# Kernel optimization log

Measured on AMD Instinct MI355X. Metric: run time of the kernel, lower is better.

Reference implementation:

```python
import jax, jax.numpy as jnp
import numpy as np

WIDTH = 16
HID = 512
NHEADS = 8
DK = HID // NHEADS
NLAYERS = 2
NHIGHWAY = 2
B = 4
S = 1024
PAD = S + 2 * WIDTH  # padded sequence length


def setup_inputs() -> dict:
    key = jax.random.key(0)
    ks = jax.random.split(key, 10)
    sc = 0.02
    f32 = jnp.float32
    return {
        "inputs": jax.random.normal(ks[0], (B, S, HID), f32),
        "masks": jnp.ones((B, S), jnp.int32),
        # 4 linears (q,k,v,out) per attention, torch Linear layout [out,in]
        "fw_lin_w": sc * jax.random.normal(ks[1], (NLAYERS, 4, HID, HID), f32),
        "fw_lin_b": jnp.zeros((NLAYERS, 4, HID), f32),
        "bw_lin_w": sc * jax.random.normal(ks[2], (NLAYERS, 4, HID, HID), f32),
        "bw_lin_b": jnp.zeros((NLAYERS, 4, HID), f32),
        # Highway: Linear(H, 2H); [:H]=nonlinear part, [H:]=gate (gate bias init 1)
        "fw_hw_w": sc * jax.random.normal(ks[3], (NLAYERS, NHIGHWAY, 2 * HID, HID), f32),
        "fw_hw_b": jnp.zeros((NLAYERS, NHIGHWAY, 2 * HID), f32).at[:, :, HID:].set(1.0),
        "bw_hw_w": sc * jax.random.normal(ks[4], (NLAYERS, NHIGHWAY, 2 * HID, HID), f32),
        "bw_hw_b": jnp.zeros((NLAYERS, NHIGHWAY, 2 * HID), f32).at[:, :, HID:].set(1.0),
        # learned boundary paddings, [width, hidden] per layer
        "fw_pad": sc * jax.random.normal(ks[5], (NLAYERS, WIDTH, HID), f32),
        "bw_pad": sc * jax.random.normal(ks[6], (NLAYERS, WIDTH, HID), f32),
        # relative-position weight vectors, [width+1] per layer
        "fw_rel": sc * jax.random.normal(ks[7], (NLAYERS, WIDTH + 1), f32),
        "bw_rel": sc * jax.random.normal(ks[8], (NLAYERS, WIDTH + 1), f32),
    }


def _band_masks():
    i = jnp.arange(PAD)[:, None]
    j = jnp.arange(PAD)[None, :]
    mf = (j <= i) & (j >= i - WIDTH - 1)          # causal band, width+2 wide
    mb = (j >= i) & (j <= i + WIDTH + 1)          # flipped (anticausal) band
    return mf, mb


def _mha(x, w, b, mask):
    # x: [B, PAD, HID]; w: [4, HID, HID]; b: [4, HID]
    def heads(t):
        return t.reshape(B, PAD, NHEADS, DK).transpose(0, 2, 1, 3)  # bhpd
    q = heads(x @ w[0].T + b[0])
    k = heads(x @ w[1].T + b[1])
    v = heads(x @ w[2].T + b[2])
    scores = jnp.einsum('bhqd,bhkd->bhqk', q, k) / np.sqrt(DK).astype(np.float32)
    scores = jnp.where(mask[None, None], scores, jnp.float32(-1e9))
    p = jax.nn.softmax(scores, axis=-1)
    o = jnp.einsum('bhqk,bhkd->bhqd', p, v)
    o = o.transpose(0, 2, 1, 3).reshape(B, PAD, HID)
    return o @ w[3].T + b[3]


def _highway(x, w, b):
    for i in range(NHIGHWAY):
        proj = x @ w[i].T + b[i]
        nonlin = jax.nn.relu(proj[..., :HID])
        gate = jax.nn.sigmoid(proj[..., HID:])
        x = gate * x + (1.0 - gate) * nonlin
    return x


def _rel(x, w, offset):
    # sum_k w[k] * x[:, offset+k : offset+k+S, :]  (width+1=17 fixed taps)
    out = w[0] * jax.lax.dynamic_slice_in_dim(x, offset, S, 1)
    for k in range(1, WIDTH + 1):
        out = out + w[k] * jax.lax.dynamic_slice_in_dim(x, offset + k, S, 1)
    return out


def _forward(inputs, fw_lin_w, fw_lin_b, bw_lin_w, bw_lin_b,
             fw_hw_w, fw_hw_b, bw_hw_w, bw_hw_b,
             fw_pad, bw_pad, fw_rel, bw_rel):
    mf, mb = _band_masks()
    f = inputs
    bk = inputs
    outs = []
    for l in range(NLAYERS):
        fp = jnp.broadcast_to(fw_pad[l][None], (B, WIDTH, HID))
        bp = jnp.broadcast_to(bw_pad[l][None], (B, WIDTH, HID))
        f_padded = jnp.concatenate([fp, f, bp], axis=1)    # [B, PAD, HID]
        b_padded = jnp.concatenate([fp, bk, bp], axis=1)
        fa = _mha(f_padded, fw_lin_w[l], fw_lin_b[l], mf)
        ba = _mha(b_padded, bw_lin_w[l], bw_lin_b[l], mb)
        # per-step: out[t] = attn[t+width] + rel-position windowed combination
        fo = fa[:, WIDTH:WIDTH + S, :] + _rel(fa, fw_rel[l], 0)
        bo = ba[:, WIDTH:WIDTH + S, :] + _rel(ba, bw_rel[l], WIDTH)
        f = _highway(fo, fw_hw_w[l], fw_hw_b[l])
        bk = _highway(bo, bw_hw_w[l], bw_hw_b[l])
        outs.append(jnp.concatenate([f, bk], axis=-1))
    return jnp.stack(outs, axis=0)  # [NLAYERS, B, S, 2*HID]


def reference(inputs, masks, fw_lin_w, fw_lin_b, bw_lin_w, bw_lin_b,
              fw_hw_w, fw_hw_b, bw_hw_w, bw_hw_b,
              fw_pad, bw_pad, fw_rel, bw_rel):
    # masks is accepted (as in the torch signature) but unused in the body
    return _forward(inputs, fw_lin_w, fw_lin_b, bw_lin_w, bw_lin_b,
                    fw_hw_w, fw_hw_b, bw_hw_w, bw_hw_b,
                    fw_pad, bw_pad, fw_rel, bw_rel)
```

## Files before the change

kernel.cpp:

```cpp
#include <hip/hip_runtime.h>

using s8 = __attribute__((ext_vector_type(8))) short;
using f4 = __attribute__((ext_vector_type(4))) float;

constexpr int WIDTH   = 16;
constexpr int HID     = 512;
constexpr int NHEADS  = 8;
constexpr int DK      = 64;
constexpr int NLAYERS = 2;
constexpr int NHW     = 2;
constexpr int B       = 4;
constexpr int S       = 1024;
constexpr int PAD     = S + 2 * WIDTH;
constexpr int RS      = 1024;
constexpr int K2      = 1024;

__device__ inline unsigned short f2bf(float x) {
    union { float f; unsigned u; } c; c.f = x;
    unsigned r = c.u + 0x7fffu + ((c.u >> 16) & 1u);
    return (unsigned short)(r >> 16);
}
__device__ inline float bf2f(unsigned short h) {
    union { float f; unsigned u; } c; c.u = ((unsigned)h) << 16; return c.f;
}
__device__ inline void split2(float x, unsigned short& h, unsigned short& l) {
    h = f2bf(x);
    l = f2bf(x - bf2f(h));
}
__device__ inline void store_split4(unsigned short* dst, float4 v) {
    unsigned short h[4], l[4];
    split2(v.x, h[0], l[0]); split2(v.y, h[1], l[1]);
    split2(v.z, h[2], l[2]); split2(v.w, h[3], l[3]);
    uint2 hp, lp;
    hp.x = h[0] | ((unsigned)h[1] << 16); hp.y = h[2] | ((unsigned)h[3] << 16);
    lp.x = l[0] | ((unsigned)l[1] << 16); lp.y = l[2] | ((unsigned)l[3] << 16);
    *(uint2*)(dst)       = hp;
    *(uint2*)(dst + 512) = lp;
}

__global__ __launch_bounds__(256) void build_pad_split(
    const float* __restrict__ src0, const float* __restrict__ src1,
    const float* __restrict__ front, const float* __restrict__ back,
    unsigned short* __restrict__ d0, unsigned short* __restrict__ d1)
{
    const float* x = blockIdx.z ? src1 : src0;
    unsigned short* xp2 = blockIdx.z ? d1 : d0;
    int idx = blockIdx.x * 256 + threadIdx.x;
    int c4 = idx & 127;
    int rest = idx >> 7;
    int p = rest % PAD;
    int b = rest / PAD;
    float4 val;
    if (p < WIDTH) {
        val = *(const float4*)(front + (size_t)p * HID + c4 * 4);
    } else if (p < WIDTH + S) {
        val = *(const float4*)(x + ((size_t)b * S + (p - WIDTH)) * HID + c4 * 4);
    } else {
        val = *(const float4*)(back + (size_t)(p - WIDTH - S) * HID + c4 * 4);
    }
    store_split4(xp2 + (size_t)(b * PAD + p) * RS + c4 * 4, val);
}

__global__ __launch_bounds__(256) void conv_w(
    const float* __restrict__ s0, const float* __restrict__ s1,
    unsigned short* __restrict__ w0, unsigned short* __restrict__ w1)
{
    const float* src = blockIdx.z ? s1 : s0;
    unsigned short* dst = blockIdx.z ? w1 : w0;
    int idx = blockIdx.x * 256 + threadIdx.x;
    int c4 = idx & 127;
    int r  = idx >> 7;
    float4 v = *(const float4*)(src + (size_t)r * HID + c4 * 4);
    store_split4(dst + (size_t)r * RS + c4 * 4, v);
}

__global__ __launch_bounds__(256) void conv_all(
    const float* __restrict__ fw_lin_w, const float* __restrict__ bw_lin_w,
    const float* __restrict__ fw_hw_w,  const float* __restrict__ bw_hw_w,
    unsigned short* __restrict__ w2all)
{
    int idx = blockIdx.x * 256 + threadIdx.x;
    int c4 = idx & 127;
    int r  = idx >> 7;
    int l  = r >> 12;
    int rr = r & 4095;
    const float* lin = blockIdx.z ? bw_lin_w : fw_lin_w;
    const float* hw  = blockIdx.z ? bw_hw_w  : fw_hw_w;
    const float* src;
    size_t drow;
    if (rr < 2048) {
        src  = lin + ((size_t)l * 2048 + rr) * HID;
        drow = (size_t)blockIdx.z * 8192 + (size_t)l * 4096 + rr;
    } else {
        int sub  = rr - 2048;
        int i_hw = sub >> 10;
        int rr2  = sub & 1023;
        int c    = rr2 & 511;
        int is_g = rr2 >> 9;
        int p    = ((c >> 4) << 5) + (c & 15) + (is_g << 4);
        src  = hw + ((size_t)l * 2048 + sub) * HID;
        drow = (size_t)blockIdx.z * 8192 + (size_t)l * 4096 + 2048 + (i_hw << 10) + p;
    }
    float4 v = *(const float4*)(src + c4 * 4);
    store_split4(w2all + drow * RS + c4 * 4, v);
}

__global__ __launch_bounds__(256) void gemm_split(
    const unsigned short* __restrict__ A0, const unsigned short* __restrict__ B0,
    const float* __restrict__ bias0, float* __restrict__ C0,
    const unsigned short* __restrict__ A1, const unsigned short* __restrict__ B1,
    const float* __restrict__ bias1, float* __restrict__ C1,
    int N)
{
    const unsigned short* A  = blockIdx.z ? A1 : A0;
    const unsigned short* Bw = blockIdx.z ? B1 : B0;
    const float* bias        = blockIdx.z ? bias1 : bias0;
    float* C                 = blockIdx.z ? C1 : C0;

    __shared__ unsigned short Als[128 * 32];
    __shared__ unsigned short Bls[128 * 32];

    const int tid  = threadIdx.x;
    const int wave = tid >> 6;
    const int lane = tid & 63;
    const int bm = blockIdx.y * 128;
    const int bn = blockIdx.x * 128;
    const int wm = (wave >> 1) * 64;
    const int wn = (wave & 1) * 64;

    const int c0 = wave * 2, c1 = wave * 2 + 1;
    const int lr = lane >> 2;
    const int kg = ((lane & 3) + (lr >> 1)) & 3;
    const int sr0 = c0 * 16 + lr;
    const int sr1 = c1 * 16 + lr;
    const int sc  = kg * 8;
    const unsigned short* Ag0 = A  + (size_t)(bm + sr0) * RS + sc;
    const unsigned short* Ag1 = A  + (size_t)(bm + sr1) * RS + sc;
    const unsigned short* Bg0 = Bw + (size_t)(bn + sr0) * RS + sc;
    const unsigned short* Bg1 = Bw + (size_t)(bn + sr1) * RS + sc;
    const int ls0 = c0 * 512;
    const int ls1 = c1 * 512;

    const int fr = lane & 15;
    const int q  = lane >> 4;
    const int rslot = (4 * fr + ((q - (fr >> 1)) & 3)) * 8;

    f4 acc[4][4] = {};

    for (int k0 = 0; k0 < K2; k0 += 32) {
        const int aoff = k0;
        const int boff = (k0 < 512) ? k0 : (k0 - 512);
        __builtin_amdgcn_global_load_lds(
            (const __attribute__((address_space(1))) void*)(Ag0 + aoff),
            (__attribute__((address_space(3))) void*)&Als[ls0], 16, 0, 0);
        __builtin_amdgcn_global_load_lds(
            (const __attribute__((address_space(1))) void*)(Ag1 + aoff),
            (__attribute__((address_space(3))) void*)&Als[ls1], 16, 0, 0);
        __builtin_amdgcn_global_load_lds(
            (const __attribute__((address_space(1))) void*)(Bg0 + boff),
            (__attribute__((address_space(3))) void*)&Bls[ls0], 16, 0, 0);
        __builtin_amdgcn_global_load_lds(
            (const __attribute__((address_space(1))) void*)(Bg1 + boff),
            (__attribute__((address_space(3))) void*)&Bls[ls1], 16, 0, 0);
        __syncthreads();

        s8 a[4], b[4];
        #pragma unroll
        for (int i = 0; i < 4; ++i)
            a[i] = *(const s8*)&Als[((wm >> 4) + i) * 512 + rslot];
        #pragma unroll
        for (int j = 0; j < 4; ++j)
            b[j] = *(const s8*)&Bls[((wn >> 4) + j) * 512 + rslot];
        #pragma unroll
        for (int i = 0; i < 4; ++i)
            #pragma unroll
            for (int j = 0; j < 4; ++j)
                acc[i][j] = __builtin_amdgcn_mfma_f32_16x16x32_bf16(
                    a[i], b[j], acc[i][j], 0, 0, 0);
        __syncthreads();
    }

    const int col = lane & 15;
    const int rb  = (lane >> 4) * 4;
    #pragma unroll
    for (int j = 0; j < 4; ++j) {
        float bj = bias[bn + wn + j * 16 + col];
        #pragma unroll
        for (int i = 0; i < 4; ++i) {
            size_t base = (size_t)(bm + wm + i * 16 + rb) * N + (bn + wn + j * 16 + col);
            #pragma unroll
            for (int r = 0; r < 4; ++r)
                C[base + (size_t)r * N] = acc[i][j][r] + bj;
        }
    }
}

__global__ __launch_bounds__(256) void gemm_hw_fused(
    const unsigned short* __restrict__ A0, const unsigned short* __restrict__ B0,
    const float* __restrict__ hwb0, unsigned short* __restrict__ o2_0,
    float* __restrict__ dst0, float* __restrict__ osl0,
    const unsigned short* __restrict__ A1, const unsigned short* __restrict__ B1,
    const float* __restrict__ hwb1, unsigned short* __restrict__ o2_1,
    float* __restrict__ dst1, float* __restrict__ osl1,
    int first)
{
    const unsigned short* A  = blockIdx.z ? A1 : A0;
    const unsigned short* Bw = blockIdx.z ? B1 : B0;
    const float* hwb         = blockIdx.z ? hwb1 : hwb0;
    unsigned short* o2       = blockIdx.z ? o2_1 : o2_0;
    float* dstf              = blockIdx.z ? dst1 : dst0;
    float* osl               = blockIdx.z ? osl1 : osl0;

    __shared__ unsigned short Als[128 * 32];
    __shared__ unsigned short Bls[128 * 32];

    const int tid  = threadIdx.x;
    const int wave = tid >> 6;
    const int lane = tid & 63;
    const int bm = blockIdx.y * 128;
    const int bn = blockIdx.x * 128;
    const int wm = (wave >> 1) * 64;
    const int wn = (wave & 1) * 64;

    const int c0 = wave * 2, c1 = wave * 2 + 1;
    const int lr = lane >> 2;
    const int kg = ((lane & 3) + (lr >> 1)) & 3;
    const int sr0 = c0 * 16 + lr;
    const int sr1 = c1 * 16 + lr;
    const int sc  = kg * 8;
    const unsigned short* Ag0 = A  + (size_t)(bm + sr0) * RS + sc;
    const unsigned short* Ag1 = A  + (size_t)(bm + sr1) * RS + sc;
    const unsigned short* Bg0 = Bw + (size_t)(bn + sr0) * RS + sc;
    const unsigned short* Bg1 = Bw + (size_t)(bn + sr1) * RS + sc;
    const int ls0 = c0 * 512;
    const int ls1 = c1 * 512;

    const int fr = lane & 15;
    const int q  = lane >> 4;
    const int rslot = (4 * fr + ((q - (fr >> 1)) & 3)) * 8;

    f4 acc[4][4] = {};

    for (int k0 = 0; k0 < K2; k0 += 32) {
        const int aoff = k0;
        const int boff = (k0 < 512) ? k0 : (k0 - 512);
        __builtin_amdgcn_global_load_lds(
            (const __attribute__((address_space(1))) void*)(Ag0 + aoff),
            (__attribute__((address_space(3))) void*)&Als[ls0], 16, 0, 0);
        __builtin_amdgcn_global_load_lds(
            (const __attribute__((address_space(1))) void*)(Ag1 + aoff),
            (__attribute__((address_space(3))) void*)&Als[ls1], 16, 0, 0);
        __builtin_amdgcn_global_load_lds(
            (const __attribute__((address_space(1))) void*)(Bg0 + boff),
            (__attribute__((address_space(3))) void*)&Bls[ls0], 16, 0, 0);
        __builtin_amdgcn_global_load_lds(
            (const __attribute__((address_space(1))) void*)(Bg1 + boff),
            (__attribute__((address_space(3))) void*)&Bls[ls1], 16, 0, 0);
        __syncthreads();

        s8 a[4], b[4];
        #pragma unroll
        for (int i = 0; i < 4; ++i)
            a[i] = *(const s8*)&Als[((wm >> 4) + i) * 512 + rslot];
        #pragma unroll
        for (int j = 0; j < 4; ++j)
            b[j] = *(const s8*)&Bls[((wn >> 4) + j) * 512 + rslot];
        #pragma unroll
        for (int i = 0; i < 4; ++i)
            #pragma unroll
            for (int j = 0; j < 4; ++j)
                acc[i][j] = __builtin_amdgcn_mfma_f32_16x16x32_bf16(
                    a[i], b[j], acc[i][j], 0, 0, 0);
        __syncthreads();
    }

    const int col = lane & 15;
    const int rb  = (lane >> 4) * 4;
    #pragma unroll
    for (int jp = 0; jp < 2; ++jp) {
        const int cc = ((bn + wn) >> 1) + jp * 16 + col;
        const float bnl = hwb[cc];
        const float bg  = hwb[512 + cc];
        #pragma unroll
        for (int i = 0; i < 4; ++i) {
            #pragma unroll
            for (int r = 0; r < 4; ++r) {
                const int row = bm + wm + i * 16 + rb + r;
                float nl = acc[i][2 * jp][r] + bnl;
                float g  = acc[i][2 * jp + 1][r] + bg;
                float xv = bf2f(A[(size_t)row * RS + cc])
                         + bf2f(A[(size_t)row * RS + cc + 512]);
                float sg = 1.f / (1.f + __expf(-g));
                float o  = sg * xv + (1.f - sg) * fmaxf(nl, 0.f);
                if (first) {
                    unsigned short hh, ll; split2(o, hh, ll);
                    o2[(size_t)row * RS + cc]       = hh;
                    o2[(size_t)row * RS + cc + 512] = ll;
                } else {
                    dstf[(size_t)row * HID + cc]      = o;
                    osl[(size_t)row * (2 * HID) + cc] = o;
                }
            }
        }
    }
}

__global__ __launch_bounds__(256) void banded_attn(
    const float* __restrict__ Q0, const float* __restrict__ Q1,
    unsigned short* __restrict__ O0, unsigned short* __restrict__ O1,
    int dir0)
{
    const float* QKV = blockIdx.z ? Q1 : Q0;
    unsigned short* O2 = blockIdx.z ? O1 : O0;
    int backward = dir0 + blockIdx.z;

    int w    = blockIdx.x * 4 + (threadIdx.x >> 6);
    int lane = threadIdx.x & 63;
    int i  = w % PAD;
    int bh = w / PAD;
    int h  = bh & (NHEADS - 1);
    int b  = bh / NHEADS;

    int jlo, n;
    if (backward) { jlo = i; n = min(WIDTH + 2, PAD - i); }
    else          { jlo = max(0, i - WIDTH - 1); n = i - jlo + 1; }

    const int s = lane >> 4;
    const int d = lane & 15;
    const size_t rowbase = (size_t)(b * PAD) * 1536;
    const int colq = h * DK;

    float4 q4 = *(const float4*)(QKV + rowbase + (size_t)i * 1536 + colq + 4 * d);

    float sc[5];
    #pragma unroll
    for (int m = 0; m < 5; ++m) {
        int t  = 4 * m + s;
        int tc = t < n ? t : n - 1;
        float4 kv = *(const float4*)(QKV + rowbase + (size_t)(jlo + tc) * 1536
                                     + 512 + colq + 4 * d);
        float p = q4.x * kv.x + q4.y * kv.y + q4.z * kv.z + q4.w * kv.w;
        p += __shfl_xor(p, 1);
        p += __shfl_xor(p, 2);
        p += __shfl_xor(p, 4);
        p += __shfl_xor(p, 8);
        sc[m] = p * 0.125f;
    }

    float sv[WIDTH + 2];
    #pragma unroll
    for (int t = 0; t < WIDTH + 2; ++t) {
        float v = __shfl(sc[t >> 2], (t & 3) << 4);
        sv[t] = (t < n) ? v : -1e30f;
    }
    float mx = sv[0];
    #pragma unroll
    for (int t = 1; t < WIDTH + 2; ++t) mx = fmaxf(mx, sv[t]);
    float denom = 0.f;
    #pragma unroll
    for (int t = 0; t < WIDTH + 2; ++t) { sv[t] = __expf(sv[t] - mx); denom += sv[t]; }
    float inv = 1.0f / denom;

    float od0 = 0.f, od1 = 0.f;
    #pragma unroll
    for (int t = 0; t < WIDTH + 2; t += 2) {
        int tc0 = t     < n ? t     : n - 1;
        int tc1 = t + 1 < n ? t + 1 : n - 1;
        od0 += sv[t]     * QKV[rowbase + (size_t)(jlo + tc0) * 1536 + 1024 + colq + lane];
        od1 += sv[t + 1] * QKV[rowbase + (size_t)(jlo + tc1) * 1536 + 1024 + colq + lane];
    }
    float od = (od0 + od1) * inv;

    unsigned short hh, ll;
    split2(od, hh, ll);
    size_t ro = (size_t)(b * PAD + i) * RS + colq + lane;
    O2[ro] = hh; O2[ro + 512] = ll;
}

__global__ __launch_bounds__(256) void rel_combine(
    const float* __restrict__ a0, const float* __restrict__ a1,
    const float* __restrict__ w0, const float* __restrict__ w1,
    unsigned short* __restrict__ f0, unsigned short* __restrict__ f1,
    int off0, int off1)
{
    const float* att = blockIdx.z ? a1 : a0;
    const float* w   = blockIdx.z ? w1 : w0;
    unsigned short* fo2 = blockIdx.z ? f1 : f0;
    int offset = blockIdx.z ? off1 : off0;

    int idx = blockIdx.x * 256 + threadIdx.x;
    int c4 = idx & 127;
    int rest = idx >> 7;
    int t = rest & (S - 1);
    int b = rest >> 10;

    const float* rowbase = att + (size_t)b * PAD * HID + c4 * 4;
    float4 acc = *(const float4*)(rowbase + (size_t)(WIDTH + t) * HID);
    #pragma unroll
    for (int k = 0; k <= WIDTH; ++k) {
        float wk = w[k];
        float4 xv = *(const float4*)(rowbase + (size_t)(offset + k + t) * HID);
        acc.x += wk * xv.x; acc.y += wk * xv.y;
        acc.z += wk * xv.z; acc.w += wk * xv.w;
    }
    store_split4(fo2 + ((size_t)b * S + t) * RS + c4 * 4, acc);
}

__global__ __launch_bounds__(256) void highway_gate(
    const unsigned short* __restrict__ x0, const unsigned short* __restrict__ x1,
    const float* __restrict__ p0, const float* __restrict__ p1,
    float* __restrict__ of0, float* __restrict__ of1,
    unsigned short* __restrict__ o20, unsigned short* __restrict__ o21,
    float* __restrict__ os0, float* __restrict__ os1)
{
    const unsigned short* x2 = blockIdx.z ? x1 : x0;
    const float* proj        = blockIdx.z ? p1 : p0;
    float* outf              = blockIdx.z ? of1 : of0;
    unsigned short* out2     = blockIdx.z ? o21 : o20;
    float* oslice            = blockIdx.z ? os1 : os0;

    int idx = blockIdx.x * 256 + threadIdx.x;
    int c4 = idx & 127;
    int r  = idx >> 7;
    const unsigned short* xr = x2 + (size_t)r * RS + c4 * 4;
    uint2 hp = *(const uint2*)(xr);
    uint2 lp = *(const uint2*)(xr + 512);
    float4 xv;
    xv.x = bf2f((unsigned short)(hp.x & 0xffff)) + bf2f((unsigned short)(lp.x & 0xffff));
    xv.y = bf2f((unsigned short)(hp.x >> 16))    + bf2f((unsigned short)(lp.x >> 16));
    xv.z = bf2f((unsigned short)(hp.y & 0xffff)) + bf2f((unsigned short)(lp.y & 0xffff));
    xv.w = bf2f((unsigned short)(hp.y >> 16))    + bf2f((unsigned short)(lp.y >> 16));

    float4 nl = *(const float4*)(proj + (size_t)r * (2 * HID) + c4 * 4);
    float4 g  = *(const float4*)(proj + (size_t)r * (2 * HID) + HID + c4 * 4);
    float4 o;
    float sg;
    sg = 1.f / (1.f + __expf(-g.x)); o.x = sg * xv.x + (1.f - sg) * fmaxf(nl.x, 0.f);
    sg = 1.f / (1.f + __expf(-g.y)); o.y = sg * xv.y + (1.f - sg) * fmaxf(nl.y, 0.f);
    sg = 1.f / (1.f + __expf(-g.z)); o.z = sg * xv.z + (1.f - sg) * fmaxf(nl.z, 0.f);
    sg = 1.f / (1.f + __expf(-g.w)); o.w = sg * xv.w + (1.f - sg) * fmaxf(nl.w, 0.f);
    if (outf)   *(float4*)(outf + (size_t)idx * 4) = o;
    if (out2)   store_split4(out2 + (size_t)r * RS + c4 * 4, o);
    if (oslice) *(float4*)(oslice + (size_t)r * (2 * HID) + c4 * 4) = o;
}

extern "C" void kernel_launch(void* const* d_in, const int* in_sizes, int n_in,
                              void* d_out, int out_size, void* d_ws, size_t ws_size,
                              hipStream_t stream)
{
    const float* inputs   = (const float*)d_in[0];
    const float* fw_lin_w = (const float*)d_in[2];
    const float* fw_lin_b = (const float*)d_in[3];
    const float* bw_lin_w = (const float*)d_in[4];
    const float* bw_lin_b = (const float*)d_in[5];
    const float* fw_hw_w  = (const float*)d_in[6];
    const float* fw_hw_b  = (const float*)d_in[7];
    const float* bw_hw_w  = (const float*)d_in[8];
    const float* bw_hw_b  = (const float*)d_in[9];
    const float* fw_pad   = (const float*)d_in[10];
    const float* bw_pad   = (const float*)d_in[11];
    const float* fw_rel   = (const float*)d_in[12];
    const float* bw_rel   = (const float*)d_in[13];
    float* out = (float*)d_out;
    float* ws  = (float*)d_ws;

    const size_t BSH  = (size_t)B * S * HID;
    const size_t QKVF = (size_t)B * PAD * 1536;
    const int MP = B * PAD;
    const int MS = B * S;

    const size_t GROUPED_FLOATS = 2 * QKVF + (2 * (size_t)MP * RS + 2 * (size_t)1536 * RS) / 2;
    const size_t WALL_FLOATS    = 2 * QKVF + (2 * (size_t)MP * RS + (size_t)2 * 8192 * RS) / 2;
    const bool wall    = ws_size >= WALL_FLOATS * 4;
    const bool grouped = wall || ws_size >= GROUPED_FLOATS * 4;
    const int G = grouped ? 2 : 1;

    float* f  = ws;
    float* bk = f + BSH;

    float* QKV[2]; float* ATT[2]; float* HWP[2];
    unsigned short* ACT2[2]; unsigned short* W2[2];
    unsigned short* ACT2B[2] = {nullptr, nullptr};
    unsigned short* w2all = nullptr;
    if (grouped) {
        QKV[0] = ws;             QKV[1] = ws + QKVF;
        float* extra = ws + 2 * BSH;
        ATT[0] = extra;          ATT[1] = extra + (size_t)MP * HID;
        HWP[0] = extra;          HWP[1] = extra + (size_t)MS * 1024;
        ACT2B[0] = (unsigned short*)extra;
        ACT2B[1] = ACT2B[0] + (size_t)MS * RS;
        unsigned short* a2 = (unsigned short*)(ws + 2 * QKVF);
        ACT2[0] = a2;            ACT2[1] = a2 + (size_t)MP * RS;
        unsigned short* w2 = a2 + 2 * (size_t)MP * RS;
        if (wall) { w2all = w2; W2[0] = W2[1] = nullptr; }
        else      { W2[0] = w2; W2[1] = w2 + (size_t)1536 * RS; }
    } else {
        float* qkvS = bk + BSH;
        QKV[0] = QKV[1] = qkvS;
        ATT[0] = ATT[1] = qkvS;
        HWP[0] = HWP[1] = qkvS;
        unsigned short* a2 = (unsigned short*)(qkvS + QKVF);
        ACT2[0] = ACT2[1] = a2;
        W2[0] = W2[1] = a2 + (size_t)MP * RS;
    }

    if (wall) {
        conv_all<<<dim3(8192 * 128 / 256, 1, 2), 256, 0, stream>>>(
            fw_lin_w, bw_lin_w, fw_hw_w, bw_hw_w, w2all);
    }
    auto WB = [&](int dir, int l, int seg) -> unsigned short* {
        return w2all + ((size_t)dir * 8192 + (size_t)l * 4096 + seg) * RS;
    };

    for (int l = 0; l < NLAYERS; ++l) {
        const float* LINW[2] = {fw_lin_w + (size_t)l * 4 * HID * HID,
                                bw_lin_w + (size_t)l * 4 * HID * HID};
        const float* LINB[2] = {fw_lin_b + (size_t)l * 4 * HID,
                                bw_lin_b + (size_t)l * 4 * HID};
        const float* HWW[2]  = {fw_hw_w + (size_t)l * NHW * 2 * HID * HID,
                                bw_hw_w + (size_t)l * NHW * 2 * HID * HID};
        const float* HWB[2]  = {fw_hw_b + (size_t)l * NHW * 2 * HID,
                                bw_hw_b + (size_t)l * NHW * 2 * HID};
        const float* RELW[2] = {fw_rel + (size_t)l * (WIDTH + 1),
                                bw_rel + (size_t)l * (WIDTH + 1)};
        const float* front = fw_pad + (size_t)l * WIDTH * HID;
        const float* back  = bw_pad + (size_t)l * WIDTH * HID;
        float* DST[2] = {f, bk};
        float* OSL[2] = {out + (size_t)l * B * S * 2 * HID,
                         out + (size_t)l * B * S * 2 * HID + HID};
        const float* SRC[2] = {(l == 0) ? inputs : f, (l == 0) ? inputs : bk};

        for (int d0 = 0; d0 < 2; d0 += G) {
            const int dB = (G == 2) ? 1 : d0;

            build_pad_split<<<dim3(MP * 128 / 256, 1, G), 256, 0, stream>>>(
                SRC[d0], SRC[dB], front, back, ACT2[0], ACT2[1]);

            unsigned short *wq0, *wq1;
            if (wall) { wq0 = WB(d0, l, 0); wq1 = WB(dB, l, 0); }
            else {
                conv_w<<<dim3(1536 * 128 / 256, 1, G), 256, 0, stream>>>(
                    LINW[d0], LINW[dB], W2[0], W2[1]);
                wq0 = W2[0]; wq1 = W2[1];
            }
            gemm_split<<<dim3(1536 / 128, MP / 128, G), 256, 0, stream>>>(
                ACT2[0], wq0, LINB[d0], QKV[0],
                ACT2[1], wq1, LINB[dB], QKV[1], 1536);

            banded_attn<<<dim3(B * NHEADS * PAD / 4, 1, G), 256, 0, stream>>>(
                QKV[0], QKV[1], ACT2[0], ACT2[1], d0);

            unsigned short *wo0, *wo1;
            if (wall) { wo0 = WB(d0, l, 1536); wo1 = WB(dB, l, 1536); }
            else {
                conv_w<<<dim3(512 * 128 / 256, 1, G), 256, 0, stream>>>(
                    LINW[d0] + 3 * (size_t)HID * HID, LINW[dB] + 3 * (size_t)HID * HID,
                    W2[0], W2[1]);
                wo0 = W2[0]; wo1 = W2[1];
            }
            gemm_split<<<dim3(512 / 128, MP / 128, G), 256, 0, stream>>>(
                ACT2[0], wo0, LINB[d0] + 3 * HID, ATT[0],
                ACT2[1], wo1, LINB[dB] + 3 * HID, ATT[1], 512);

            rel_combine<<<dim3(MS * 128 / 256, 1, G), 256, 0, stream>>>(
                ATT[0], ATT[1], RELW[d0], RELW[dB], ACT2[0], ACT2[1],
                d0 * WIDTH, dB * WIDTH);

            if (wall) {
                gemm_hw_fused<<<dim3(1024 / 128, MS / 128, G), 256, 0, stream>>>(
                    ACT2[0], WB(d0, l, 2048), HWB[d0], ACT2B[0], nullptr, nullptr,
                    ACT2[1], WB(dB, l, 2048), HWB[dB], ACT2B[1], nullptr, nullptr, 1);
                gemm_hw_fused<<<dim3(1024 / 128, MS / 128, G), 256, 0, stream>>>(
                    ACT2B[0], WB(d0, l, 3072), HWB[d0] + 1024, nullptr, DST[d0], OSL[d0],
                    ACT2B[1], WB(dB, l, 3072), HWB[dB] + 1024, nullptr, DST[dB], OSL[dB], 0);
            } else {
                for (int i = 0; i < NHW; ++i) {
                    conv_w<<<dim3(1024 * 128 / 256, 1, G), 256, 0, stream>>>(
                        HWW[d0] + (size_t)i * 2 * HID * HID,
                        HWW[dB] + (size_t)i * 2 * HID * HID, W2[0], W2[1]);
                    gemm_split<<<dim3(1024 / 128, MS / 128, G), 256, 0, stream>>>(
                        ACT2[0], W2[0], HWB[d0] + (size_t)i * 2 * HID, HWP[0],
                        ACT2[1], W2[1], HWB[dB] + (size_t)i * 2 * HID, HWP[1], 1024);
                    const bool last = (i == NHW - 1);
                    highway_gate<<<dim3(MS * 128 / 256, 1, G), 256, 0, stream>>>(
                        ACT2[0], ACT2[1], HWP[0], HWP[1],
                        last ? DST[d0] : (float*)nullptr,
                        last ? DST[dB] : (float*)nullptr,
                        last ? (unsigned short*)nullptr : ACT2[0],
                        last ? (unsigned short*)nullptr : ACT2[1],
                        last ? OSL[d0] : (float*)nullptr,
                        last ? OSL[dB] : (float*)nullptr);
                }
            }
        }
    }
}
```

Before: 563.6 us.

## Triple-buffer LDS pipeline with XCD-aware block swizzle in split GEMMs

Both bf16-split GEMM kernels now use a three-slot LDS ring. Global-to-LDS loads for k-step t+2 are issued before the MFMAs for step t, with vmcnt waits and a single barrier per iteration in place of two __syncthreads. The MFMA block is wrapped in s_setprio, and block indices are remapped so that neighbouring tiles land on the same XCD, which should improve L2 reuse. This triples the LDS footprint to 48KB per block, which may lower occupancy, and it depends on correct vmcnt accounting for the in-flight stages.

```diff
diff --git a/kernel.cpp b/kernel.cpp
--- a/kernel.cpp
+++ b/kernel.cpp
@@ -36,6 +36,17 @@
     lp.x = l[0] | ((unsigned)l[1] << 16); lp.y = l[2] | ((unsigned)l[3] << 16);
     *(uint2*)(dst)       = hp;
     *(uint2*)(dst + 512) = lp;
+}
+
+__device__ inline void xcd_swizzle(int& bx, int& by) {
+    const int gx = gridDim.x, gy = gridDim.y;
+    const int nwg = gx * gy;
+    const int orig = by * gx + bx;
+    const int q = nwg >> 3, r = nwg & 7;
+    const int x8 = orig & 7, i8 = orig >> 3;
+    const int wg = (x8 < r ? x8 * (q + 1) : r * (q + 1) + (x8 - r) * q) + i8;
+    bx = wg % gx;
+    by = wg / gx;
 }
 
 __global__ __launch_bounds__(256) void build_pad_split(
@@ -117,14 +128,16 @@
     const float* bias        = blockIdx.z ? bias1 : bias0;
     float* C                 = blockIdx.z ? C1 : C0;
 
-    __shared__ unsigned short Als[128 * 32];
-    __shared__ unsigned short Bls[128 * 32];
+    __shared__ unsigned short Als[3][128 * 32];
+    __shared__ unsigned short Bls[3][128 * 32];
 
     const int tid  = threadIdx.x;
     const int wave = tid >> 6;
     const int lane = tid & 63;
-    const int bm = blockIdx.y * 128;
-    const int bn = blockIdx.x * 128;
+    int bx = blockIdx.x, by = blockIdx.y;
+    xcd_swizzle(bx, by);
+    const int bm = by * 128;
+    const int bn = bx * 128;
     const int wm = (wave >> 1) * 64;
     const int wn = (wave & 1) * 64;
 
@@ -147,38 +160,58 @@
 
     f4 acc[4][4] = {};
 
-    for (int k0 = 0; k0 < K2; k0 += 32) {
+    auto stage = [&](int slot, int k0) {
         const int aoff = k0;
         const int boff = (k0 < 512) ? k0 : (k0 - 512);
         __builtin_amdgcn_global_load_lds(
             (const __attribute__((address_space(1))) void*)(Ag0 + aoff),
-            (__attribute__((address_space(3))) void*)&Als[ls0], 16, 0, 0);
+            (__attribute__((address_space(3))) void*)&Als[slot][ls0], 16, 0, 0);
         __builtin_amdgcn_global_load_lds(
             (const __attribute__((address_space(1))) void*)(Ag1 + aoff),
-            (__attribute__((address_space(3))) void*)&Als[ls1], 16, 0, 0);
+            (__attribute__((address_space(3))) void*)&Als[slot][ls1], 16, 0, 0);
         __builtin_amdgcn_global_load_lds(
             (const __attribute__((address_space(1))) void*)(Bg0 + boff),
-            (__attribute__((address_space(3))) void*)&Bls[ls0], 16, 0, 0);
+            (__attribute__((address_space(3))) void*)&Bls[slot][ls0], 16, 0, 0);
         __builtin_amdgcn_global_load_lds(
             (const __attribute__((address_space(1))) void*)(Bg1 + boff),
-            (__attribute__((address_space(3))) void*)&Bls[ls1], 16, 0, 0);
-        __syncthreads();
-
+            (__attribute__((address_space(3))) void*)&Bls[slot][ls1], 16, 0, 0);
+    };
+    auto compute = [&](int slot) {
         s8 a[4], b[4];
         #pragma unroll
         for (int i = 0; i < 4; ++i)
-            a[i] = *(const s8*)&Als[((wm >> 4) + i) * 512 + rslot];
+            a[i] = *(const s8*)&Als[slot][((wm >> 4) + i) * 512 + rslot];
         #pragma unroll
         for (int j = 0; j < 4; ++j)
-            b[j] = *(const s8*)&Bls[((wn >> 4) + j) * 512 + rslot];
+            b[j] = *(const s8*)&Bls[slot][((wn >> 4) + j) * 512 + rslot];
+        __builtin_amdgcn_s_setprio(1);
         #pragma unroll
         for (int i = 0; i < 4; ++i)
             #pragma unroll
             for (int j = 0; j < 4; ++j)
                 acc[i][j] = __builtin_amdgcn_mfma_f32_16x16x32_bf16(
                     a[i], b[j], acc[i][j], 0, 0, 0);
-        __syncthreads();
-    }
+        __builtin_amdgcn_s_setprio(0);
+    };
+
+    stage(0, 0);
+    stage(1, 32);
+    int rs_ = 0, ss_ = 2;
+    #pragma unroll 1
+    for (int t = 0; t < 30; ++t) {
+        asm volatile("s_waitcnt vmcnt(4)" ::: "memory");
+        __builtin_amdgcn_s_barrier();
+        stage(ss_, (t + 2) * 32);
+        compute(rs_);
+        rs_ = (rs_ == 2) ? 0 : rs_ + 1;
+        ss_ = (ss_ == 2) ? 0 : ss_ + 1;
+    }
+    asm volatile("s_waitcnt vmcnt(4)" ::: "memory");
+    __builtin_amdgcn_s_barrier();
+    compute(0);
+    asm volatile("s_waitcnt vmcnt(0)" ::: "memory");
+    __builtin_amdgcn_s_barrier();
+    compute(1);
 
     const int col = lane & 15;
     const int rb  = (lane >> 4) * 4;
@@ -211,14 +244,16 @@
     float* dstf              = blockIdx.z ? dst1 : dst0;
     float* osl               = blockIdx.z ? osl1 : osl0;
 
-    __shared__ unsigned short Als[128 * 32];
-    __shared__ unsigned short Bls[128 * 32];
+    __shared__ unsigned short Als[3][128 * 32];
+    __shared__ unsigned short Bls[3][128 * 32];
 
     const int tid  = threadIdx.x;
     const int wave = tid >> 6;
     const int lane = tid & 63;
-    const int bm = blockIdx.y * 128;
-    const int bn = blockIdx.x * 128;
+    int bx = blockIdx.x, by = blockIdx.y;
+    xcd_swizzle(bx, by);
+    const int bm = by * 128;
+    const int bn = bx * 128;
     const int wm = (wave >> 1) * 64;
     const int wn = (wave & 1) * 64;
 
@@ -241,38 +276,58 @@
 
     f4 acc[4][4] = {};
 
-    for (int k0 = 0; k0 < K2; k0 += 32) {
+    auto stage = [&](int slot, int k0) {
         const int aoff = k0;
         const int boff = (k0 < 512) ? k0 : (k0 - 512);
         __builtin_amdgcn_global_load_lds(
             (const __attribute__((address_space(1))) void*)(Ag0 + aoff),
-            (__attribute__((address_space(3))) void*)&Als[ls0], 16, 0, 0);
+            (__attribute__((address_space(3))) void*)&Als[slot][ls0], 16, 0, 0);
         __builtin_amdgcn_global_load_lds(
             (const __attribute__((address_space(1))) void*)(Ag1 + aoff),
-            (__attribute__((address_space(3))) void*)&Als[ls1], 16, 0, 0);
+            (__attribute__((address_space(3))) void*)&Als[slot][ls1], 16, 0, 0);
         __builtin_amdgcn_global_load_lds(
             (const __attribute__((address_space(1))) void*)(Bg0 + boff),
-            (__attribute__((address_space(3))) void*)&Bls[ls0], 16, 0, 0);
+            (__attribute__((address_space(3))) void*)&Bls[slot][ls0], 16, 0, 0);
         __builtin_amdgcn_global_load_lds(
             (const __attribute__((address_space(1))) void*)(Bg1 + boff),
-            (__attribute__((address_space(3))) void*)&Bls[ls1], 16, 0, 0);
-        __syncthreads();
-
+            (__attribute__((address_space(3))) void*)&Bls[slot][ls1], 16, 0, 0);
+    };
+    auto compute = [&](int slot) {
         s8 a[4], b[4];
         #pragma unroll
         for (int i = 0; i < 4; ++i)
-            a[i] = *(const s8*)&Als[((wm >> 4) + i) * 512 + rslot];
+            a[i] = *(const s8*)&Als[slot][((wm >> 4) + i) * 512 + rslot];
         #pragma unroll
         for (int j = 0; j < 4; ++j)
-            b[j] = *(const s8*)&Bls[((wn >> 4) + j) * 512 + rslot];
+            b[j] = *(const s8*)&Bls[slot][((wn >> 4) + j) * 512 + rslot];
+        __builtin_amdgcn_s_setprio(1);
         #pragma unroll
         for (int i = 0; i < 4; ++i)
             #pragma unroll
             for (int j = 0; j < 4; ++j)
                 acc[i][j] = __builtin_amdgcn_mfma_f32_16x16x32_bf16(
                     a[i], b[j], acc[i][j], 0, 0, 0);
-        __syncthreads();
-    }
+        __builtin_amdgcn_s_setprio(0);
+    };
+
+    stage(0, 0);
+    stage(1, 32);
+    int rs_ = 0, ss_ = 2;
+    #pragma unroll 1
+    for (int t = 0; t < 30; ++t) {
+        asm volatile("s_waitcnt vmcnt(4)" ::: "memory");
+        __builtin_amdgcn_s_barrier();
+        stage(ss_, (t + 2) * 32);
+        compute(rs_);
+        rs_ = (rs_ == 2) ? 0 : rs_ + 1;
+        ss_ = (ss_ == 2) ? 0 : ss_ + 1;
+    }
+    asm volatile("s_waitcnt vmcnt(4)" ::: "memory");
+    __builtin_amdgcn_s_barrier();
+    compute(0);
+    asm volatile("s_waitcnt vmcnt(0)" ::: "memory");
+    __builtin_amdgcn_s_barrier();
+    compute(1);
 
     const int col = lane & 15;
     const int rb  = (lane >> 4) * 4;
```

Measured after the change: 564.1 us. Within noise of the previous version (+0.1%).

## Triple-buffer GEMM LDS pipeline with 128x256 tiles, 8 waves, XCD swizzle

Applied to the files above, without the earlier changes.

Rewrites the shared GEMM main loop as a three-stage LDS ring: global_load_lds for tile kt+2 is issued while tile kt is consumed, with explicit vmcnt waits and raw s_barrier in place of two __syncthreads per step. Block tiles grow to 128x256 with 512 threads (8 waves), and blocks are remapped so consecutive tiles land on the same XCD for L2 reuse. The cost targeted is load latency that was previously exposed each k-step, plus redundant B traffic across XCDs. In exchange the kernels use more LDS per block, launch fewer and larger blocks, and drop the old bank-conflict-avoiding LDS slot permutation.

```diff
diff --git a/kernel.cpp b/kernel.cpp
--- a/kernel.cpp
+++ b/kernel.cpp
@@ -36,6 +36,17 @@
     lp.x = l[0] | ((unsigned)l[1] << 16); lp.y = l[2] | ((unsigned)l[3] << 16);
     *(uint2*)(dst)       = hp;
     *(uint2*)(dst + 512) = lp;
+}
+
+__device__ inline void xcd_swizzle(int& bx, int& by) {
+    const int gx = gridDim.x, gy = gridDim.y;
+    const int nwg = gx * gy;
+    const int orig = by * gx + bx;
+    const int q = nwg >> 3, r = nwg & 7;
+    const int x8 = orig & 7, i8 = orig >> 3;
+    const int wg = (x8 < r ? x8 * (q + 1) : r * (q + 1) + (x8 - r) * q) + i8;
+    bx = wg % gx;
+    by = wg / gx;
 }
 
 __global__ __launch_bounds__(256) void build_pad_split(
@@ -105,7 +116,72 @@
     store_split4(w2all + drow * RS + c4 * 4, v);
 }
 
-__global__ __launch_bounds__(256) void gemm_split(
+#define GEMM8_PREAMBLE                                                          \
+    __shared__ unsigned short Als[3][128 * 32];                                 \
+    __shared__ unsigned short Bls[3][256 * 32];                                 \
+    const int tid  = threadIdx.x;                                               \
+    const int wave = tid >> 6;                                                  \
+    const int lane = tid & 63;                                                  \
+    int bx = blockIdx.x, by = blockIdx.y;                                       \
+    xcd_swizzle(bx, by);                                                        \
+    const int bm = by * 128;                                                    \
+    const int bn = bx * 256;                                                    \
+    const int wm = (wave >> 2) * 64;                                            \
+    const int wn = (wave & 3) * 64;                                             \
+    const int srow = wave * 16 + (lane >> 2);      \
+    const int sslot = (lane & 3) * 8;              \
+    const unsigned short* Asrc  = A  + (size_t)(bm + srow) * RS + sslot;        \
+    const unsigned short* Bsrc0 = Bw + (size_t)(bn + srow) * RS + sslot;        \
+    const unsigned short* Bsrc1 = Bw + (size_t)(bn + 128 + srow) * RS + sslot;  \
+    const int fr = lane & 15;                                                   \
+    const int q  = lane >> 4;                                                   \
+    f4 acc[4][4] = {};                                                          \
+    auto stage = [&](int buf, int kt) {                                         \
+        const int aoff = kt * 32;                                               \
+        const int boff = (kt < 16) ? aoff : (aoff - 512);                       \
+        __builtin_amdgcn_global_load_lds(                                       \
+            (const __attribute__((address_space(1))) void*)(Asrc + aoff),       \
+            (__attribute__((address_space(3))) void*)&Als[buf][wave * 512],     \
+            16, 0, 0);                                                          \
+        __builtin_amdgcn_global_load_lds(                                       \
+            (const __attribute__((address_space(1))) void*)(Bsrc0 + boff),      \
+            (__attribute__((address_space(3))) void*)&Bls[buf][wave * 512],     \
+            16, 0, 0);                                                          \
+        __builtin_amdgcn_global_load_lds(                                       \
+            (const __attribute__((address_space(1))) void*)(Bsrc1 + boff),      \
+            (__attribute__((address_space(3))) void*)&Bls[buf][4096 + wave * 512], \
+            16, 0, 0);                                                          \
+    };                                                                          \
+    stage(0, 0);                                                                \
+    stage(1, 1);                                                                \
+    asm volatile("s_waitcnt vmcnt(3)" ::: "memory");                            \
+    asm volatile("s_barrier" ::: "memory");                                     \
+    _Pragma("unroll")                                                           \
+    for (int kt = 0; kt < 32; ++kt) {                                           \
+        const int buf = kt % 3;                                                 \
+        s8 a[4], b[4];                                                          \
+        _Pragma("unroll")                                                       \
+        for (int i = 0; i < 4; ++i)                                             \
+            a[i] = *(const s8*)&Als[buf][(wm + i * 16 + fr) * 32 + q * 8];      \
+        _Pragma("unroll")                                                       \
+        for (int j = 0; j < 4; ++j)                                             \
+            b[j] = *(const s8*)&Bls[buf][(wn + j * 16 + fr) * 32 + q * 8];      \
+        if (kt + 2 < 32) stage((kt + 2) % 3, kt + 2);                           \
+        if (kt < 30)       asm volatile("s_waitcnt vmcnt(3)" ::: "memory");     \
+        else if (kt == 30) asm volatile("s_waitcnt vmcnt(0)" ::: "memory");     \
+        asm volatile("s_barrier" ::: "memory");                                 \
+        __builtin_amdgcn_s_setprio(1);                                          \
+        _Pragma("unroll")                                                       \
+        for (int i = 0; i < 4; ++i)                                             \
+            _Pragma("unroll")                                                   \
+            for (int j = 0; j < 4; ++j)                                         \
+                acc[i][j] = __builtin_amdgcn_mfma_f32_16x16x32_bf16(            \
+                    a[i], b[j], acc[i][j], 0, 0, 0);                            \
+        __builtin_amdgcn_s_setprio(0);                                          \
+        if (kt < 31) asm volatile("s_barrier" ::: "memory");                    \
+    }
+
+__global__ __launch_bounds__(512, 4) void gemm_split(
     const unsigned short* __restrict__ A0, const unsigned short* __restrict__ B0,
     const float* __restrict__ bias0, float* __restrict__ C0,
     const unsigned short* __restrict__ A1, const unsigned short* __restrict__ B1,
@@ -117,68 +193,7 @@
     const float* bias        = blockIdx.z ? bias1 : bias0;
     float* C                 = blockIdx.z ? C1 : C0;
 
-    __shared__ unsigned short Als[128 * 32];
-    __shared__ unsigned short Bls[128 * 32];
-
-    const int tid  = threadIdx.x;
-    const int wave = tid >> 6;
-    const int lane = tid & 63;
-    const int bm = blockIdx.y * 128;
-    const int bn = blockIdx.x * 128;
-    const int wm = (wave >> 1) * 64;
-    const int wn = (wave & 1) * 64;
-
-    const int c0 = wave * 2, c1 = wave * 2 + 1;
-    const int lr = lane >> 2;
-    const int kg = ((lane & 3) + (lr >> 1)) & 3;
-    const int sr0 = c0 * 16 + lr;
-    const int sr1 = c1 * 16 + lr;
-    const int sc  = kg * 8;
-    const unsigned short* Ag0 = A  + (size_t)(bm + sr0) * RS + sc;
-    const unsigned short* Ag1 = A  + (size_t)(bm + sr1) * RS + sc;
-    const unsigned short* Bg0 = Bw + (size_t)(bn + sr0) * RS + sc;
-    const unsigned short* Bg1 = Bw + (size_t)(bn + sr1) * RS + sc;
-    const int ls0 = c0 * 512;
-    const int ls1 = c1 * 512;
-
-    const int fr = lane & 15;
-    const int q  = lane >> 4;
-    const int rslot = (4 * fr + ((q - (fr >> 1)) & 3)) * 8;
-
-    f4 acc[4][4] = {};
-
-    for (int k0 = 0; k0 < K2; k0 += 32) {
-        const int aoff = k0;
-        const int boff = (k0 < 512) ? k0 : (k0 - 512);
-        __builtin_amdgcn_global_load_lds(
-            (const __attribute__((address_space(1))) void*)(Ag0 + aoff),
-            (__attribute__((address_space(3))) void*)&Als[ls0], 16, 0, 0);
-        __builtin_amdgcn_global_load_lds(
-            (const __attribute__((address_space(1))) void*)(Ag1 + aoff),
-            (__attribute__((address_space(3))) void*)&Als[ls1], 16, 0, 0);
-        __builtin_amdgcn_global_load_lds(
-            (const __attribute__((address_space(1))) void*)(Bg0 + boff),
-            (__attribute__((address_space(3))) void*)&Bls[ls0], 16, 0, 0);
-        __builtin_amdgcn_global_load_lds(
-            (const __attribute__((address_space(1))) void*)(Bg1 + boff),
-            (__attribute__((address_space(3))) void*)&Bls[ls1], 16, 0, 0);
-        __syncthreads();
-
-        s8 a[4], b[4];
-        #pragma unroll
-        for (int i = 0; i < 4; ++i)
-            a[i] = *(const s8*)&Als[((wm >> 4) + i) * 512 + rslot];
-        #pragma unroll
-        for (int j = 0; j < 4; ++j)
-            b[j] = *(const s8*)&Bls[((wn >> 4) + j) * 512 + rslot];
-        #pragma unroll
-        for (int i = 0; i < 4; ++i)
-            #pragma unroll
-            for (int j = 0; j < 4; ++j)
-                acc[i][j] = __builtin_amdgcn_mfma_f32_16x16x32_bf16(
-                    a[i], b[j], acc[i][j], 0, 0, 0);
-        __syncthreads();
-    }
+    GEMM8_PREAMBLE
 
     const int col = lane & 15;
     const int rb  = (lane >> 4) * 4;
@@ -195,7 +210,7 @@
     }
 }
 
-__global__ __launch_bounds__(256) void gemm_hw_fused(
+__global__ __launch_bounds__(512, 4) void gemm_hw_fused(
     const unsigned short* __restrict__ A0, const unsigned short* __restrict__ B0,
     const float* __restrict__ hwb0, unsigned short* __restrict__ o2_0,
     float* __restrict__ dst0, float* __restrict__ osl0,
@@ -211,68 +226,7 @@
     float* dstf              = blockIdx.z ? dst1 : dst0;
     float* osl               = blockIdx.z ? osl1 : osl0;
 
-    __shared__ unsigned short Als[128 * 32];
-    __shared__ unsigned short Bls[128 * 32];
-
-    const int tid  = threadIdx.x;
-    const int wave = tid >> 6;
-    const int lane = tid & 63;
-    const int bm = blockIdx.y * 128;
-    const int bn = blockIdx.x * 128;
-    const int wm = (wave >> 1) * 64;
-    const int wn = (wave & 1) * 64;
-
-    const int c0 = wave * 2, c1 = wave * 2 + 1;
-    const int lr = lane >> 2;
-    const int kg = ((lane & 3) + (lr >> 1)) & 3;
-    const int sr0 = c0 * 16 + lr;
-    const int sr1 = c1 * 16 + lr;
-    const int sc  = kg * 8;
-    const unsigned short* Ag0 = A  + (size_t)(bm + sr0) * RS + sc;
-    const unsigned short* Ag1 = A  + (size_t)(bm + sr1) * RS + sc;
-    const unsigned short* Bg0 = Bw + (size_t)(bn + sr0) * RS + sc;
-    const unsigned short* Bg1 = Bw + (size_t)(bn + sr1) * RS + sc;
-    const int ls0 = c0 * 512;
-    const int ls1 = c1 * 512;
-
-    const int fr = lane & 15;
-    const int q  = lane >> 4;
-    const int rslot = (4 * fr + ((q - (fr >> 1)) & 3)) * 8;
-
-    f4 acc[4][4] = {};
-
-    for (int k0 = 0; k0 < K2; k0 += 32) {
-        const int aoff = k0;
-        const int boff = (k0 < 512) ? k0 : (k0 - 512);
-        __builtin_amdgcn_global_load_lds(
-            (const __attribute__((address_space(1))) void*)(Ag0 + aoff),
-            (__attribute__((address_space(3))) void*)&Als[ls0], 16, 0, 0);
-        __builtin_amdgcn_global_load_lds(
-            (const __attribute__((address_space(1))) void*)(Ag1 + aoff),
-            (__attribute__((address_space(3))) void*)&Als[ls1], 16, 0, 0);
-        __builtin_amdgcn_global_load_lds(
-            (const __attribute__((address_space(1))) void*)(Bg0 + boff),
-            (__attribute__((address_space(3))) void*)&Bls[ls0], 16, 0, 0);
-        __builtin_amdgcn_global_load_lds(
-            (const __attribute__((address_space(1))) void*)(Bg1 + boff),
-            (__attribute__((address_space(3))) void*)&Bls[ls1], 16, 0, 0);
-        __syncthreads();
-
-        s8 a[4], b[4];
-        #pragma unroll
-        for (int i = 0; i < 4; ++i)
-            a[i] = *(const s8*)&Als[((wm >> 4) + i) * 512 + rslot];
-        #pragma unroll
-        for (int j = 0; j < 4; ++j)
-            b[j] = *(const s8*)&Bls[((wn >> 4) + j) * 512 + rslot];
-        #pragma unroll
-        for (int i = 0; i < 4; ++i)
-            #pragma unroll
-            for (int j = 0; j < 4; ++j)
-                acc[i][j] = __builtin_amdgcn_mfma_f32_16x16x32_bf16(
-                    a[i], b[j], acc[i][j], 0, 0, 0);
-        __syncthreads();
-    }
+    GEMM8_PREAMBLE
 
     const int col = lane & 15;
     const int rb  = (lane >> 4) * 4;
@@ -543,7 +497,7 @@
                     LINW[d0], LINW[dB], W2[0], W2[1]);
                 wq0 = W2[0]; wq1 = W2[1];
             }
-            gemm_split<<<dim3(1536 / 128, MP / 128, G), 256, 0, stream>>>(
+            gemm_split<<<dim3(1536 / 256, MP / 128, G), 512, 0, stream>>>(
                 ACT2[0], wq0, LINB[d0], QKV[0],
                 ACT2[1], wq1, LINB[dB], QKV[1], 1536);
 
@@ -558,7 +512,7 @@
                     W2[0], W2[1]);
                 wo0 = W2[0]; wo1 = W2[1];
             }
-            gemm_split<<<dim3(512 / 128, MP / 128, G), 256, 0, stream>>>(
+            gemm_split<<<dim3(512 / 256, MP / 128, G), 512, 0, stream>>>(
                 ACT2[0], wo0, LINB[d0] + 3 * HID, ATT[0],
                 ACT2[1], wo1, LINB[dB] + 3 * HID, ATT[1], 512);
 
@@ -567,10 +521,10 @@
                 d0 * WIDTH, dB * WIDTH);
 
             if (wall) {
-                gemm_hw_fused<<<dim3(1024 / 128, MS / 128, G), 256, 0, stream>>>(
+                gemm_hw_fused<<<dim3(1024 / 256, MS / 128, G), 512, 0, stream>>>(
                     ACT2[0], WB(d0, l, 2048), HWB[d0], ACT2B[0], nullptr, nullptr,
                     ACT2[1], WB(dB, l, 2048), HWB[dB], ACT2B[1], nullptr, nullptr, 1);
-                gemm_hw_fused<<<dim3(1024 / 128, MS / 128, G), 256, 0, stream>>>(
+                gemm_hw_fused<<<dim3(1024 / 256, MS / 128, G), 512, 0, stream>>>(
                     ACT2B[0], WB(d0, l, 3072), HWB[d0] + 1024, nullptr, DST[d0], OSL[d0],
                     ACT2B[1], WB(dB, l, 3072), HWB[dB] + 1024, nullptr, DST[dB], OSL[dB], 0);
             } else {
@@ -578,7 +532,7 @@
                     conv_w<<<dim3(1024 * 128 / 256, 1, G), 256, 0, stream>>>(
                         HWW[d0] + (size_t)i * 2 * HID * HID,
                         HWW[dB] + (size_t)i * 2 * HID * HID, W2[0], W2[1]);
-                    gemm_split<<<dim3(1024 / 128, MS / 128, G), 256, 0, stream>>>(
+                    gemm_split<<<dim3(1024 / 256, MS / 128, G), 512, 0, stream>>>(
                         ACT2[0], W2[0], HWB[d0] + (size_t)i * 2 * HID, HWP[0],
                         ACT2[1], W2[1], HWB[dB] + (size_t)i * 2 * HID, HWP[1], 1024);
                     const bool last = (i == NHW - 1);
```

Measured after the change: 619.5 us. +9.9%, slower.
